# Kernel optimization log

Hardware: AMD Instinct MI355X
Metric: run time of the kernel (lower is better)

Reference implementation:

```python
import jax, jax.numpy as jnp
import numpy as np

B, T = 2048, 512
H1, H2, H3 = 100, 60, 30


def _glorot(key, shape, fan):
    bound = 1.0 / np.sqrt(fan)
    return jax.random.uniform(key, shape, jnp.float32, -bound, bound)


def setup_inputs() -> dict:
    key = jax.random.key(0)
    ks = jax.random.split(key, 17)
    inp = {"x": jax.random.normal(ks[0], (B, T, 2), jnp.float32)}
    # layer 1: input 2 -> hidden 100
    inp["W_ih1"] = _glorot(ks[1], (H1, 2), H1)
    inp["W_hh1"] = _glorot(ks[2], (H1, H1), H1)
    inp["b_ih1"] = _glorot(ks[3], (H1,), H1)
    inp["b_hh1"] = _glorot(ks[4], (H1,), H1)
    # layer 2: 100 -> 60
    inp["W_ih2"] = _glorot(ks[5], (H2, H1), H2)
    inp["W_hh2"] = _glorot(ks[6], (H2, H2), H2)
    inp["b_ih2"] = _glorot(ks[7], (H2,), H2)
    inp["b_hh2"] = _glorot(ks[8], (H2,), H2)
    # layer 3: 60 -> 30
    inp["W_ih3"] = _glorot(ks[9], (H3, H2), H3)
    inp["W_hh3"] = _glorot(ks[10], (H3, H3), H3)
    inp["b_ih3"] = _glorot(ks[11], (H3,), H3)
    inp["b_hh3"] = _glorot(ks[12], (H3,), H3)
    # heads
    inp["W_o1"] = _glorot(ks[13], (10, H3), 10)
    inp["b_o1"] = _glorot(ks[14], (10,), 10)
    inp["W_o2"] = _glorot(ks[15], (2, 10), 2)
    inp["b_o2"] = _glorot(ks[16], (2,), 2)
    return inp


def rnn_layer(x, W_ih, W_hh, b_ih, b_hh):
    # x: [B, T, in]; precompute the time-parallel input projection once
    xp = jnp.einsum("bti,hi->bth", x, W_ih) + (b_ih + b_hh)  # [B, T, H]
    h0 = jnp.zeros((x.shape[0], W_hh.shape[0]), x.dtype)

    def step(h, xt):  # xt: [B, H]
        h = jnp.tanh(xt + h @ W_hh.T)
        return h, h

    _, ys = jax.lax.scan(step, h0, jnp.swapaxes(xp, 0, 1))  # [T, B, H]
    return jnp.swapaxes(ys, 0, 1)  # [B, T, H]


def reference(x, W_ih1, W_hh1, b_ih1, b_hh1, W_ih2, W_hh2, b_ih2, b_hh2,
              W_ih3, W_hh3, b_ih3, b_hh3, W_o1, b_o1, W_o2, b_o2):
    h = rnn_layer(x, W_ih1, W_hh1, b_ih1, b_hh1)
    h = rnn_layer(h, W_ih2, W_hh2, b_ih2, b_hh2)
    h = rnn_layer(h, W_ih3, W_hh3, b_ih3, b_hh3)
    o = jnp.einsum("bth,oh->bto", h, W_o1) + b_o1
    return jnp.einsum("bto,po->btp", o, W_o2) + b_o2  # [B, T, 2]
```

## Files before the change

### kernel.cpp

```cpp
#include <hip/hip_runtime.h>

typedef _Float16 v8hf __attribute__((ext_vector_type(8)));
typedef float    v4f  __attribute__((ext_vector_type(4)));

#define MFMA16(a, b, c) __builtin_amdgcn_mfma_f32_16x16x32_f16((a), (b), (c), 0, 0, 0)

#define TT 512
#define BT 16
#define NTH 512

#define PBLK  8192u
#define H2OFF 4352u
#define H3OFF 6656u
#define XSTO  16384u
#define RINGO 49152u

__shared__ __align__(64) char SM[57344];

__device__ __forceinline__ v4f tanh4(v4f r) {
    const float KS = 2.8853900817779268f;
    const float CL = 13.8498724f;
    float z0 = __builtin_amdgcn_fmed3f(r[0] * KS, -CL, CL);
    float z1 = __builtin_amdgcn_fmed3f(r[1] * KS, -CL, CL);
    float z2 = __builtin_amdgcn_fmed3f(r[2] * KS, -CL, CL);
    float z3 = __builtin_amdgcn_fmed3f(r[3] * KS, -CL, CL);
    float a0 = __builtin_amdgcn_exp2f(z0) + 1.f;
    float a1 = __builtin_amdgcn_exp2f(z1) + 1.f;
    float a2 = __builtin_amdgcn_exp2f(z2) + 1.f;
    float a3 = __builtin_amdgcn_exp2f(z3) + 1.f;
    float P = a0 * a1, Q = a2 * a3;
    float R = __builtin_amdgcn_rcpf(P * Q);
    float iP = Q * R, iQ = P * R;
    v4f t;
    t[0] = 1.f - 2.f * (a1 * iP);
    t[1] = 1.f - 2.f * (a0 * iP);
    t[2] = 1.f - 2.f * (a3 * iQ);
    t[3] = 1.f - 2.f * (a2 * iQ);
    return t;
}

__global__ __launch_bounds__(NTH)
void rnn3_hl(const float* __restrict__ xg,
             const float* __restrict__ Wih1, const float* __restrict__ Whh1,
             const float* __restrict__ bih1, const float* __restrict__ bhh1,
             const float* __restrict__ Wih2, const float* __restrict__ Whh2,
             const float* __restrict__ bih2, const float* __restrict__ bhh2,
             const float* __restrict__ Wih3, const float* __restrict__ Whh3,
             const float* __restrict__ bih3, const float* __restrict__ bhh3,
             const float* __restrict__ Wo1,  const float* __restrict__ bo1,
             const float* __restrict__ Wo2,  const float* __restrict__ bo2,
             float* __restrict__ outg)
{
    const int tid   = threadIdx.x;
    const int lane  = tid & 63;
    const int wid   = tid >> 6;
    const int col   = lane & 15;
    const int g     = lane >> 4;
    const int bbase = blockIdx.x * BT;

    {
        float4 z = {0.f, 0.f, 0.f, 0.f};
        float4* p4 = (float4*)SM;
        for (int i = tid; i < 1024; i += NTH) p4[i] = z;
        for (int i = tid; i < BT * TT * 2; i += NTH) {
            float v = xg[(size_t)bbase * (TT * 2) + i];
            int b = i >> 10, r = i & 1023, t = r >> 1, c = r & 1;
            *(_Float16*)(SM + XSTO + (unsigned)t * 64u + (unsigned)b * 4u + (unsigned)c * 2u) = (_Float16)v;
        }
    }

    v8hf F[14];
    #pragma unroll
    for (int i = 0; i < 14; ++i) F[i] = (v8hf)(_Float16)0.f;
    float bb0 = 0.f, bb1 = 0.f, bb2 = 0.f;

    auto ldW = [&](const float* W, int rows, int cols, int j, int kt) -> v8hf {
        v8hf r;
        #pragma unroll
        for (int e = 0; e < 8; ++e) {
            const int k = kt * 32 + g * 8 + e;
            float v = (j < rows && k < cols) ? W[j * cols + k] : 0.f;
            r[e] = (_Float16)v;
        }
        return r;
    };
    auto ldW1 = [&](int j, int kt) -> v8hf {
        v8hf r;
        #pragma unroll
        for (int e = 0; e < 8; ++e) {
            const int k = kt * 32 + g * 8 + e;
            float v = 0.f;
            if (j < 100) {
                if (k < 100)       v = Whh1[j * 100 + k];
                else if (k == 112) v = Wih1[j * 2];
                else if (k == 113) v = Wih1[j * 2 + 1];
            }
            r[e] = (_Float16)v;
        }
        return r;
    };
    auto bL1 = [&](int j) -> float { return (j < 100) ? bih1[j] + bhh1[j] : 0.f; };
    auto bL2 = [&](int j) -> float { return (j < 60) ? bih2[j] + bhh2[j] : 0.f; };
    auto bL3 = [&](int j) -> float { return (j < 30) ? bih3[j] + bhh3[j] : 0.f; };

    unsigned oA = 0, oB = 0, oC = 0, oW1 = 0, oW2 = 0, oW3 = 0, oXw = 0, oRw = 0;

    if (wid < 4) {
        const int jA = 16 * wid + col;
        #pragma unroll
        for (int kt = 0; kt < 4; ++kt) {
            F[0 + kt] = ldW1(jA, kt);
            F[8 + kt] = ldW(Wih2, 60, 100, jA, kt);
        }
        F[12] = ldW(Whh2, 60, 60, jA, 0);
        F[13] = ldW(Whh2, 60, 60, jA, 1);
        bb0 = bL1(jA); bb2 = bL2(jA);
        if (wid < 3) {
            const int jB = jA + 64;
            #pragma unroll
            for (int kt = 0; kt < 4; ++kt) F[4 + kt] = ldW1(jB, kt);
            bb1 = bL1(jB);
        }
        oA  = (unsigned)col * 272u + (unsigned)g * 16u;
        oB  = PBLK + H2OFF + (unsigned)col * 144u + (unsigned)g * 16u;
        oW1 = PBLK + (unsigned)(4 * g) * 272u + (unsigned)jA * 2u;
        oW2 = H2OFF + (unsigned)(4 * g) * 144u + (unsigned)jA * 2u;
        oXw = PBLK + (unsigned)lane * 272u + 224u;
    } else if (wid < 6) {
        const int j3 = 16 * (wid - 4) + col;
        F[0] = ldW(Wih3, 30, 60, j3, 0);
        F[1] = ldW(Wih3, 30, 60, j3, 1);
        F[2] = ldW(Whh3, 30, 30, j3, 0);
        bb0 = bL3(j3);
        oB  = PBLK + H2OFF + (unsigned)col * 144u + (unsigned)g * 16u;
        oC  = H3OFF + (unsigned)col * 80u + (unsigned)g * 16u;
        oW3 = PBLK + H3OFF + (unsigned)(4 * g) * 80u + (unsigned)j3 * 2u;
    } else if (wid == 6) {
        #pragma unroll
        for (int e = 0; e < 8; ++e) {
            const int k = g * 8 + e;
            float v = 0.f;
            if (col < 2 && k < 30) {
                #pragma unroll
                for (int u = 0; u < 10; ++u) v += Wo2[col * 10 + u] * Wo1[u * 30 + k];
            }
            F[0][e] = (_Float16)v;
        }
        if (col < 2) {
            float bv = bo2[col];
            #pragma unroll
            for (int u = 0; u < 10; ++u) bv += Wo2[col * 10 + u] * bo1[u];
            bb0 = bv;
        }
        oC  = H3OFF + (unsigned)col * 80u + (unsigned)g * 16u;
        oRw = RINGO + (unsigned)(4 * g) * 512u + (unsigned)col * 4u;
    }

    __syncthreads();
    if (tid < BT)
        *(unsigned*)(SM + (unsigned)tid * 272u + 224u) =
            *(const unsigned*)(SM + XSTO + (unsigned)tid * 4u);
    __syncthreads();

#define ST_H1(r, EX) { \
    *(_Float16*)(SM + oW1 + (EX) + 0u)   = (_Float16)(r)[0]; \
    *(_Float16*)(SM + oW1 + (EX) + 272u) = (_Float16)(r)[1]; \
    *(_Float16*)(SM + oW1 + (EX) + 544u) = (_Float16)(r)[2]; \
    *(_Float16*)(SM + oW1 + (EX) + 816u) = (_Float16)(r)[3]; }
#define ST_H2(r) { \
    *(_Float16*)(SM + oW2 + 0u)   = (_Float16)(r)[0]; \
    *(_Float16*)(SM + oW2 + 144u) = (_Float16)(r)[1]; \
    *(_Float16*)(SM + oW2 + 288u) = (_Float16)(r)[2]; \
    *(_Float16*)(SM + oW2 + 432u) = (_Float16)(r)[3]; }
#define ST_H3(r) { \
    *(_Float16*)(SM + oW3 + 0u)   = (_Float16)(r)[0]; \
    *(_Float16*)(SM + oW3 + 80u)  = (_Float16)(r)[1]; \
    *(_Float16*)(SM + oW3 + 160u) = (_Float16)(r)[2]; \
    *(_Float16*)(SM + oW3 + 240u) = (_Float16)(r)[3]; }

    for (int s = 0; s < TT + 4; ++s) {
        if (wid < 4) {
            if (wid == 3 && lane < BT && s < TT - 1) {
                unsigned xv = *(const unsigned*)(SM + XSTO + (unsigned)(s + 1) * 64u + (unsigned)lane * 4u);
                *(unsigned*)(SM + oXw) = xv;
            }
            if (s <= TT) {
                v8hf A0 = *(const v8hf*)(SM + oA);
                v8hf A1 = *(const v8hf*)(SM + oA + 64u);
                v8hf A2 = *(const v8hf*)(SM + oA + 128u);
                v8hf A3 = *(const v8hf*)(SM + oA + 192u);
                v8hf B0 = *(const v8hf*)(SM + oB);
                v8hf B1 = *(const v8hf*)(SM + oB + 64u);
                if (s < TT) {
                    {
                        v4f p = {bb0, bb0, bb0, bb0}, q = {0.f, 0.f, 0.f, 0.f};
                        p = MFMA16(A0, F[0], p); q = MFMA16(A1, F[1], q);
                        p = MFMA16(A2, F[2], p); q = MFMA16(A3, F[3], q);
                        v4f r = tanh4(p + q); ST_H1(r, 0u);
                    }
                    if (wid < 3) {
                        v4f p = {bb1, bb1, bb1, bb1}, q = {0.f, 0.f, 0.f, 0.f};
                        p = MFMA16(A0, F[4], p); q = MFMA16(A1, F[5], q);
                        p = MFMA16(A2, F[6], p); q = MFMA16(A3, F[7], q);
                        v4f r = tanh4(p + q); ST_H1(r, 128u);
                    }
                }
                if (s >= 1) {
                    v4f p = {bb2, bb2, bb2, bb2}, q = {0.f, 0.f, 0.f, 0.f};
                    p = MFMA16(A0, F[8],  p); q = MFMA16(A1, F[9],  q);
                    p = MFMA16(A2, F[10], p); q = MFMA16(A3, F[11], q);
                    p = MFMA16(B0, F[12], p); q = MFMA16(B1, F[13], q);
                    v4f r = tanh4(p + q); ST_H2(r);
                }
            }
            oA ^= PBLK; oB ^= PBLK; oW1 ^= PBLK; oW2 ^= PBLK; oXw ^= PBLK;
        } else if (wid < 6) {
            if (s >= 2 && s <= TT + 1) {
                v8hf B0 = *(const v8hf*)(SM + oB);
                v8hf B1 = *(const v8hf*)(SM + oB + 64u);
                v8hf C0 = *(const v8hf*)(SM + oC);
                v4f p = {bb0, bb0, bb0, bb0}, q = {0.f, 0.f, 0.f, 0.f};
                p = MFMA16(B0, F[0], p); q = MFMA16(B1, F[1], q);
                p = MFMA16(C0, F[2], p);
                v4f r = tanh4(p + q); ST_H3(r);
            }
            oB ^= PBLK; oC ^= PBLK; oW3 ^= PBLK;
        } else if (wid == 6) {
            if (s >= 3 && s <= TT + 2) {
                v8hf C0 = *(const v8hf*)(SM + oC);
                v4f o = {bb0, bb0, bb0, bb0};
                o = MFMA16(C0, F[0], o);
                const unsigned so = ((unsigned)(s - 3) & 63u) * 8u;
                if (col < 2) {
                    *(float*)(SM + oRw + so + 0u)    = o[0];
                    *(float*)(SM + oRw + so + 512u)  = o[1];
                    *(float*)(SM + oRw + so + 1024u) = o[2];
                    *(float*)(SM + oRw + so + 1536u) = o[3];
                }
            }
            oC ^= PBLK;
        } else {
            if (s >= 35 && ((s - 4) & 31) == 31) {
                const int tbase = s - 35;
                const unsigned rb = RINGO + (((unsigned)tbase & 63u) >> 1) * 16u;
                #pragma unroll
                for (int jj = 0; jj < 4; ++jj) {
                    const int f = lane + 64 * jj;
                    const int b = f >> 4, k = f & 15;
                    float4 v = *(const float4*)(SM + rb + (unsigned)b * 512u + (unsigned)k * 16u);
                    *(float4*)(outg + ((size_t)(bbase + b) * TT + tbase) * 2 + 4 * k) = v;
                }
            }
        }
        __syncthreads();
    }
}

extern "C" void kernel_launch(void* const* d_in, const int* in_sizes, int n_in,
                              void* d_out, int out_size, void* d_ws, size_t ws_size,
                              hipStream_t stream) {
    (void)in_sizes; (void)n_in; (void)d_ws; (void)ws_size; (void)out_size;
    const float* x     = (const float*)d_in[0];
    const float* W_ih1 = (const float*)d_in[1];
    const float* W_hh1 = (const float*)d_in[2];
    const float* b_ih1 = (const float*)d_in[3];
    const float* b_hh1 = (const float*)d_in[4];
    const float* W_ih2 = (const float*)d_in[5];
    const float* W_hh2 = (const float*)d_in[6];
    const float* b_ih2 = (const float*)d_in[7];
    const float* b_hh2 = (const float*)d_in[8];
    const float* W_ih3 = (const float*)d_in[9];
    const float* W_hh3 = (const float*)d_in[10];
    const float* b_ih3 = (const float*)d_in[11];
    const float* b_hh3 = (const float*)d_in[12];
    const float* W_o1  = (const float*)d_in[13];
    const float* b_o1  = (const float*)d_in[14];
    const float* W_o2  = (const float*)d_in[15];
    const float* b_o2  = (const float*)d_in[16];
    float* out = (float*)d_out;

    rnn3_hl<<<2048 / BT, NTH, 0, stream>>>(
        x, W_ih1, W_hh1, b_ih1, b_hh1,
        W_ih2, W_hh2, b_ih2, b_hh2,
        W_ih3, W_hh3, b_ih3, b_hh3,
        W_o1, b_o1, W_o2, b_o2, out);
}
```

Before: 311.5 us.

## Specialise time loop into unrolled ping-pong phases and prioritise layer-1/2 waves

The 516-step time loop is unrolled by two with compile-time buffer parity, and prologue/epilogue steps are split out so per-step conditionals and pointer XORs disappear. The x-staging copy moves from wave 3 (on the critical layer-1 path) to the head wave 6. Waves running layers 1 and 2 get raised scheduling priority via s_setprio. This trades larger code size and more register pressure for less per-step scalar and branch overhead on the serial recurrence.

```diff
diff --git a/kernel.cpp b/kernel.cpp
--- a/kernel.cpp
+++ b/kernel.cpp
@@ -40,7 +40,7 @@
 }
 
 __global__ __launch_bounds__(NTH)
-void rnn3_hl(const float* __restrict__ xg,
+void rnn3_sp(const float* __restrict__ xg,
              const float* __restrict__ Wih1, const float* __restrict__ Whh1,
              const float* __restrict__ bih1, const float* __restrict__ bhh1,
              const float* __restrict__ Wih2, const float* __restrict__ Whh2,
@@ -103,7 +103,8 @@
     auto bL2 = [&](int j) -> float { return (j < 60) ? bih2[j] + bhh2[j] : 0.f; };
     auto bL3 = [&](int j) -> float { return (j < 30) ? bih3[j] + bhh3[j] : 0.f; };
 
-    unsigned oA = 0, oB = 0, oC = 0, oW1 = 0, oW2 = 0, oW3 = 0, oXw = 0, oRw = 0;
+    unsigned bRd = 0, bRd2 = 0, bRd3 = 0, bW1 = 0, bW2 = 0, bW3 = 0, bXw = 0, bRw = 0;
+    unsigned xr = 0;
 
     if (wid < 4) {
         const int jA = 16 * wid + col;
@@ -121,20 +122,19 @@
             for (int kt = 0; kt < 4; ++kt) F[4 + kt] = ldW1(jB, kt);
             bb1 = bL1(jB);
         }
-        oA  = (unsigned)col * 272u + (unsigned)g * 16u;
-        oB  = PBLK + H2OFF + (unsigned)col * 144u + (unsigned)g * 16u;
-        oW1 = PBLK + (unsigned)(4 * g) * 272u + (unsigned)jA * 2u;
-        oW2 = H2OFF + (unsigned)(4 * g) * 144u + (unsigned)jA * 2u;
-        oXw = PBLK + (unsigned)lane * 272u + 224u;
+        bRd  = (unsigned)col * 272u + (unsigned)g * 16u;
+        bRd2 = (unsigned)col * 144u + (unsigned)g * 16u;
+        bW1  = (unsigned)(4 * g) * 272u + (unsigned)jA * 2u;
+        bW2  = (unsigned)(4 * g) * 144u + (unsigned)jA * 2u;
     } else if (wid < 6) {
         const int j3 = 16 * (wid - 4) + col;
         F[0] = ldW(Wih3, 30, 60, j3, 0);
         F[1] = ldW(Wih3, 30, 60, j3, 1);
         F[2] = ldW(Whh3, 30, 30, j3, 0);
         bb0 = bL3(j3);
-        oB  = PBLK + H2OFF + (unsigned)col * 144u + (unsigned)g * 16u;
-        oC  = H3OFF + (unsigned)col * 80u + (unsigned)g * 16u;
-        oW3 = PBLK + H3OFF + (unsigned)(4 * g) * 80u + (unsigned)j3 * 2u;
+        bRd2 = (unsigned)col * 144u + (unsigned)g * 16u;
+        bRd3 = (unsigned)col * 80u + (unsigned)g * 16u;
+        bW3  = (unsigned)(4 * g) * 80u + (unsigned)j3 * 2u;
     } else if (wid == 6) {
         #pragma unroll
         for (int e = 0; e < 8; ++e) {
@@ -152,8 +152,10 @@
             for (int u = 0; u < 10; ++u) bv += Wo2[col * 10 + u] * bo1[u];
             bb0 = bv;
         }
-        oC  = H3OFF + (unsigned)col * 80u + (unsigned)g * 16u;
-        oRw = RINGO + (unsigned)(4 * g) * 512u + (unsigned)col * 4u;
+        bRd3 = (unsigned)col * 80u + (unsigned)g * 16u;
+        bXw  = (unsigned)lane * 272u + 224u;
+        xr   = XSTO + 64u + (unsigned)lane * 4u;
+        bRw  = RINGO + (unsigned)(4 * g) * 512u + (unsigned)col * 4u;
     }
 
     __syncthreads();
@@ -162,98 +164,116 @@
             *(const unsigned*)(SM + XSTO + (unsigned)tid * 4u);
     __syncthreads();
 
-#define ST_H1(r, EX) { \
-    *(_Float16*)(SM + oW1 + (EX) + 0u)   = (_Float16)(r)[0]; \
-    *(_Float16*)(SM + oW1 + (EX) + 272u) = (_Float16)(r)[1]; \
-    *(_Float16*)(SM + oW1 + (EX) + 544u) = (_Float16)(r)[2]; \
-    *(_Float16*)(SM + oW1 + (EX) + 816u) = (_Float16)(r)[3]; }
-#define ST_H2(r) { \
-    *(_Float16*)(SM + oW2 + 0u)   = (_Float16)(r)[0]; \
-    *(_Float16*)(SM + oW2 + 144u) = (_Float16)(r)[1]; \
-    *(_Float16*)(SM + oW2 + 288u) = (_Float16)(r)[2]; \
-    *(_Float16*)(SM + oW2 + 432u) = (_Float16)(r)[3]; }
-#define ST_H3(r) { \
-    *(_Float16*)(SM + oW3 + 0u)   = (_Float16)(r)[0]; \
-    *(_Float16*)(SM + oW3 + 80u)  = (_Float16)(r)[1]; \
-    *(_Float16*)(SM + oW3 + 160u) = (_Float16)(r)[2]; \
-    *(_Float16*)(SM + oW3 + 240u) = (_Float16)(r)[3]; }
-
-    for (int s = 0; s < TT + 4; ++s) {
-        if (wid < 4) {
-            if (wid == 3 && lane < BT && s < TT - 1) {
-                unsigned xv = *(const unsigned*)(SM + XSTO + (unsigned)(s + 1) * 64u + (unsigned)lane * 4u);
-                *(unsigned*)(SM + oXw) = xv;
-            }
-            if (s <= TT) {
-                v8hf A0 = *(const v8hf*)(SM + oA);
-                v8hf A1 = *(const v8hf*)(SM + oA + 64u);
-                v8hf A2 = *(const v8hf*)(SM + oA + 128u);
-                v8hf A3 = *(const v8hf*)(SM + oA + 192u);
-                v8hf B0 = *(const v8hf*)(SM + oB);
-                v8hf B1 = *(const v8hf*)(SM + oB + 64u);
-                if (s < TT) {
-                    {
-                        v4f p = {bb0, bb0, bb0, bb0}, q = {0.f, 0.f, 0.f, 0.f};
-                        p = MFMA16(A0, F[0], p); q = MFMA16(A1, F[1], q);
-                        p = MFMA16(A2, F[2], p); q = MFMA16(A3, F[3], q);
-                        v4f r = tanh4(p + q); ST_H1(r, 0u);
-                    }
-                    if (wid < 3) {
-                        v4f p = {bb1, bb1, bb1, bb1}, q = {0.f, 0.f, 0.f, 0.f};
-                        p = MFMA16(A0, F[4], p); q = MFMA16(A1, F[5], q);
-                        p = MFMA16(A2, F[6], p); q = MFMA16(A3, F[7], q);
-                        v4f r = tanh4(p + q); ST_H1(r, 128u);
-                    }
-                }
-                if (s >= 1) {
-                    v4f p = {bb2, bb2, bb2, bb2}, q = {0.f, 0.f, 0.f, 0.f};
-                    p = MFMA16(A0, F[8],  p); q = MFMA16(A1, F[9],  q);
-                    p = MFMA16(A2, F[10], p); q = MFMA16(A3, F[11], q);
-                    p = MFMA16(B0, F[12], p); q = MFMA16(B1, F[13], q);
-                    v4f r = tanh4(p + q); ST_H2(r);
-                }
-            }
-            oA ^= PBLK; oB ^= PBLK; oW1 ^= PBLK; oW2 ^= PBLK; oXw ^= PBLK;
-        } else if (wid < 6) {
-            if (s >= 2 && s <= TT + 1) {
-                v8hf B0 = *(const v8hf*)(SM + oB);
-                v8hf B1 = *(const v8hf*)(SM + oB + 64u);
-                v8hf C0 = *(const v8hf*)(SM + oC);
-                v4f p = {bb0, bb0, bb0, bb0}, q = {0.f, 0.f, 0.f, 0.f};
-                p = MFMA16(B0, F[0], p); q = MFMA16(B1, F[1], q);
-                p = MFMA16(C0, F[2], p);
-                v4f r = tanh4(p + q); ST_H3(r);
-            }
-            oB ^= PBLK; oC ^= PBLK; oW3 ^= PBLK;
-        } else if (wid == 6) {
-            if (s >= 3 && s <= TT + 2) {
-                v8hf C0 = *(const v8hf*)(SM + oC);
-                v4f o = {bb0, bb0, bb0, bb0};
-                o = MFMA16(C0, F[0], o);
-                const unsigned so = ((unsigned)(s - 3) & 63u) * 8u;
-                if (col < 2) {
-                    *(float*)(SM + oRw + so + 0u)    = o[0];
-                    *(float*)(SM + oRw + so + 512u)  = o[1];
-                    *(float*)(SM + oRw + so + 1024u) = o[2];
-                    *(float*)(SM + oRw + so + 1536u) = o[3];
-                }
-            }
-            oC ^= PBLK;
-        } else {
-            if (s >= 35 && ((s - 4) & 31) == 31) {
-                const int tbase = s - 35;
-                const unsigned rb = RINGO + (((unsigned)tbase & 63u) >> 1) * 16u;
-                #pragma unroll
-                for (int jj = 0; jj < 4; ++jj) {
-                    const int f = lane + 64 * jj;
-                    const int b = f >> 4, k = f & 15;
-                    float4 v = *(const float4*)(SM + rb + (unsigned)b * 512u + (unsigned)k * 16u);
-                    *(float4*)(outg + ((size_t)(bbase + b) * TT + tbase) * 2 + 4 * k) = v;
-                }
-            }
-        }
-        __syncthreads();
+    if (wid < 4) __builtin_amdgcn_s_setprio(1);
+
+    auto flushfn = [&](int s) {
+        const int tbase = s - 35;
+        const unsigned rb = RINGO + (((unsigned)tbase & 63u) >> 1) * 16u;
+        #pragma unroll
+        for (int jj = 0; jj < 4; ++jj) {
+            const int f = lane + 64 * jj;
+            const int b = f >> 4, k = f & 15;
+            float4 v = *(const float4*)(SM + rb + (unsigned)b * 512u + (unsigned)k * 16u);
+            *(float4*)(outg + ((size_t)(bbase + b) * TT + tbase) * 2 + 4 * k) = v;
+        }
+    };
+
+#define PHASE(RP, L1ON, L2ON, L3ON, HDON, XON, S) do {                                   \
+    const unsigned RB_ = (RP) ? PBLK : 0u;                                               \
+    const unsigned WB_ = (RP) ? 0u : PBLK;                                               \
+    if (wid < 4) {                                                                       \
+        if ((L1ON) || (L2ON)) {                                                          \
+            v8hf A0 = *(const v8hf*)(SM + bRd + RB_ + 0u);                               \
+            v8hf A1 = *(const v8hf*)(SM + bRd + RB_ + 64u);                              \
+            v8hf A2 = *(const v8hf*)(SM + bRd + RB_ + 128u);                             \
+            v8hf A3 = *(const v8hf*)(SM + bRd + RB_ + 192u);                             \
+            if (L1ON) {                                                                  \
+                { v4f p = {bb0, bb0, bb0, bb0}, q = {0.f, 0.f, 0.f, 0.f};                \
+                  p = MFMA16(A0, F[0], p); q = MFMA16(A1, F[1], q);                      \
+                  p = MFMA16(A2, F[2], p); q = MFMA16(A3, F[3], q);                      \
+                  v4f r = tanh4(p + q);                                                  \
+                  *(_Float16*)(SM + bW1 + WB_ + 0u)   = (_Float16)r[0];                  \
+                  *(_Float16*)(SM + bW1 + WB_ + 272u) = (_Float16)r[1];                  \
+                  *(_Float16*)(SM + bW1 + WB_ + 544u) = (_Float16)r[2];                  \
+                  *(_Float16*)(SM + bW1 + WB_ + 816u) = (_Float16)r[3]; }                \
+                if (wid < 3) {                                                           \
+                  v4f p = {bb1, bb1, bb1, bb1}, q = {0.f, 0.f, 0.f, 0.f};                \
+                  p = MFMA16(A0, F[4], p); q = MFMA16(A1, F[5], q);                      \
+                  p = MFMA16(A2, F[6], p); q = MFMA16(A3, F[7], q);                      \
+                  v4f r = tanh4(p + q);                                                  \
+                  *(_Float16*)(SM + bW1 + WB_ + 128u)  = (_Float16)r[0];                 \
+                  *(_Float16*)(SM + bW1 + WB_ + 400u)  = (_Float16)r[1];                 \
+                  *(_Float16*)(SM + bW1 + WB_ + 672u)  = (_Float16)r[2];                 \
+                  *(_Float16*)(SM + bW1 + WB_ + 944u)  = (_Float16)r[3]; }               \
+            }                                                                            \
+            if (L2ON) {                                                                  \
+                v8hf B0 = *(const v8hf*)(SM + bRd2 + WB_ + H2OFF + 0u);                  \
+                v8hf B1 = *(const v8hf*)(SM + bRd2 + WB_ + H2OFF + 64u);                 \
+                v4f p = {bb2, bb2, bb2, bb2}, q = {0.f, 0.f, 0.f, 0.f};                  \
+                p = MFMA16(A0, F[8],  p); q = MFMA16(A1, F[9],  q);                      \
+                p = MFMA16(A2, F[10], p); q = MFMA16(A3, F[11], q);                      \
+                p = MFMA16(B0, F[12], p); q = MFMA16(B1, F[13], q);                      \
+                v4f r = tanh4(p + q);                                                    \
+                *(_Float16*)(SM + bW2 + RB_ + H2OFF + 0u)   = (_Float16)r[0];            \
+                *(_Float16*)(SM + bW2 + RB_ + H2OFF + 144u) = (_Float16)r[1];            \
+                *(_Float16*)(SM + bW2 + RB_ + H2OFF + 288u) = (_Float16)r[2];            \
+                *(_Float16*)(SM + bW2 + RB_ + H2OFF + 432u) = (_Float16)r[3];            \
+            }                                                                            \
+        }                                                                                \
+    } else if (wid < 6) {                                                                \
+        if (L3ON) {                                                                      \
+            v8hf B0 = *(const v8hf*)(SM + bRd2 + WB_ + H2OFF + 0u);                      \
+            v8hf B1 = *(const v8hf*)(SM + bRd2 + WB_ + H2OFF + 64u);                     \
+            v8hf C0 = *(const v8hf*)(SM + bRd3 + RB_ + H3OFF);                           \
+            v4f p = {bb0, bb0, bb0, bb0}, q = {0.f, 0.f, 0.f, 0.f};                      \
+            p = MFMA16(B0, F[0], p); q = MFMA16(B1, F[1], q);                            \
+            p = MFMA16(C0, F[2], p);                                                     \
+            v4f r = tanh4(p + q);                                                        \
+            *(_Float16*)(SM + bW3 + WB_ + H3OFF + 0u)   = (_Float16)r[0];                \
+            *(_Float16*)(SM + bW3 + WB_ + H3OFF + 80u)  = (_Float16)r[1];                \
+            *(_Float16*)(SM + bW3 + WB_ + H3OFF + 160u) = (_Float16)r[2];                \
+            *(_Float16*)(SM + bW3 + WB_ + H3OFF + 240u) = (_Float16)r[3];                \
+        }                                                                                \
+    } else if (wid == 6) {                                                               \
+        if (XON) {                                                                       \
+            if (lane < 16) {                                                             \
+                unsigned xv = *(const unsigned*)(SM + xr);                               \
+                *(unsigned*)(SM + bXw + WB_) = xv;                                       \
+            }                                                                            \
+        }                                                                                \
+        xr += 64u;                                                                       \
+        if (HDON) {                                                                      \
+            v8hf C0 = *(const v8hf*)(SM + bRd3 + RB_ + H3OFF);                           \
+            v4f o = {bb0, bb0, bb0, bb0};                                                \
+            o = MFMA16(C0, F[0], o);                                                     \
+            const unsigned so = (((unsigned)(S) - 3u) & 63u) * 8u;                       \
+            if (col < 2) {                                                               \
+                *(float*)(SM + bRw + so + 0u)    = o[0];                                 \
+                *(float*)(SM + bRw + so + 512u)  = o[1];                                 \
+                *(float*)(SM + bRw + so + 1024u) = o[2];                                 \
+                *(float*)(SM + bRw + so + 1536u) = o[3];                                 \
+            }                                                                            \
+        }                                                                                \
+    } else {                                                                             \
+        if ((S) >= 35 && (((S) - 4) & 31) == 31) flushfn((S));                           \
+    }                                                                                    \
+    __syncthreads();                                                                     \
+} while (0)
+
+    PHASE(0, 1, 0, 0, 0, 1, 0);
+    PHASE(1, 1, 1, 0, 0, 1, 1);
+    PHASE(0, 1, 1, 1, 0, 1, 2);
+    PHASE(1, 1, 1, 1, 1, 1, 3);
+    for (int s = 4; s < 510; s += 2) {
+        PHASE(0, 1, 1, 1, 1, 1, s);
+        PHASE(1, 1, 1, 1, 1, 1, s + 1);
     }
+    PHASE(0, 1, 1, 1, 1, 1, 510);
+    PHASE(1, 1, 1, 1, 1, 0, 511);
+    PHASE(0, 0, 1, 1, 1, 0, 512);
+    PHASE(1, 0, 0, 1, 1, 0, 513);
+    PHASE(0, 0, 0, 0, 1, 0, 514);
+    PHASE(1, 0, 0, 0, 0, 0, 515);
 }
 
 extern "C" void kernel_launch(void* const* d_in, const int* in_sizes, int n_in,
@@ -279,7 +299,7 @@
     const float* b_o2  = (const float*)d_in[16];
     float* out = (float*)d_out;
 
-    rnn3_hl<<<2048 / BT, NTH, 0, stream>>>(
+    rnn3_sp<<<2048 / BT, NTH, 0, stream>>>(
         x, W_ih1, W_hh1, b_ih1, b_hh1,
         W_ih2, W_hh2, b_ih2, b_hh2,
         W_ih3, W_hh3, b_ih3, b_hh3,
```

Result: no change. 307.5 us (-1.3%).

## Assign one wavefront per RNN layer with register-resident state and two-step barriers

Applied to the files above, without the earlier changes.

Restructures the kernel so each of four wavefronts owns one role: layer 1, layer 2, layer 3 plus the fused output head, and the output writer. Hidden state now stays in registers as MFMA B-operands, with the transposed MFMA operand order letting outputs pack straight into the next step's input. Each barrier covers two timesteps, using 4-deep shared rings between layers. The tanh scale factor is folded into the weights and biases. This cuts the block-wide barriers and shared-memory round trips on the recurrent path, but one wavefront now serially carries all 28 layer-1 MFMAs per step, which lengthens the critical path.

```diff
diff --git a/kernel.cpp b/kernel.cpp
--- a/kernel.cpp
+++ b/kernel.cpp
@@ -7,23 +7,23 @@
 
 #define TT 512
 #define BT 16
-#define NTH 512
-
-#define PBLK  8192u
-#define H2OFF 4352u
-#define H3OFF 6656u
-#define XSTO  16384u
-#define RINGO 49152u
-
-__shared__ __align__(64) char SM[57344];
-
-__device__ __forceinline__ v4f tanh4(v4f r) {
-    const float KS = 2.8853900817779268f;
-    const float CL = 13.8498724f;
-    float z0 = __builtin_amdgcn_fmed3f(r[0] * KS, -CL, CL);
-    float z1 = __builtin_amdgcn_fmed3f(r[1] * KS, -CL, CL);
-    float z2 = __builtin_amdgcn_fmed3f(r[2] * KS, -CL, CL);
-    float z3 = __builtin_amdgcn_fmed3f(r[3] * KS, -CL, CL);
+#define NTH 256
+#define KS 2.8853900817779268f
+#define CL 13.8498724f
+
+#define H1R 0u
+#define H2R 16384u
+#define XST 24576u
+#define ORG 57408u
+#define SMEMB 65600
+
+extern __shared__ __align__(16) char SM[];
+
+__device__ __forceinline__ v4f tanh4s(v4f z) {
+    float z0 = __builtin_amdgcn_fmed3f(z[0], -CL, CL);
+    float z1 = __builtin_amdgcn_fmed3f(z[1], -CL, CL);
+    float z2 = __builtin_amdgcn_fmed3f(z[2], -CL, CL);
+    float z3 = __builtin_amdgcn_fmed3f(z[3], -CL, CL);
     float a0 = __builtin_amdgcn_exp2f(z0) + 1.f;
     float a1 = __builtin_amdgcn_exp2f(z1) + 1.f;
     float a2 = __builtin_amdgcn_exp2f(z2) + 1.f;
@@ -39,8 +39,19 @@
     return t;
 }
 
-__global__ __launch_bounds__(NTH)
-void rnn3_hl(const float* __restrict__ xg,
+__device__ __forceinline__ unsigned pk2h(float a, float b) {
+    union { _Float16 h[2]; unsigned u; } x;
+    x.h[0] = (_Float16)a; x.h[1] = (_Float16)b;
+    return x.u;
+}
+__device__ __forceinline__ v8hf mk8(unsigned a, unsigned b, unsigned c, unsigned d) {
+    union { unsigned u[4]; v8hf h; } x;
+    x.u[0] = a; x.u[1] = b; x.u[2] = c; x.u[3] = d;
+    return x.h;
+}
+
+__global__ __launch_bounds__(NTH, 1)
+void rnn3_ws(const float* __restrict__ xg,
              const float* __restrict__ Wih1, const float* __restrict__ Whh1,
              const float* __restrict__ bih1, const float* __restrict__ bhh1,
              const float* __restrict__ Wih2, const float* __restrict__ Whh2,
@@ -58,191 +69,202 @@
     const int g     = lane >> 4;
     const int bbase = blockIdx.x * BT;
 
-    {
-        float4 z = {0.f, 0.f, 0.f, 0.f};
-        float4* p4 = (float4*)SM;
-        for (int i = tid; i < 1024; i += NTH) p4[i] = z;
-        for (int i = tid; i < BT * TT * 2; i += NTH) {
-            float v = xg[(size_t)bbase * (TT * 2) + i];
-            int b = i >> 10, r = i & 1023, t = r >> 1, c = r & 1;
-            *(_Float16*)(SM + XSTO + (unsigned)t * 64u + (unsigned)b * 4u + (unsigned)c * 2u) = (_Float16)v;
-        }
+    for (int i = tid; i < BT * TT; i += NTH) {
+        const int b = i >> 9, t = i & 511;
+        float2 xv = *(const float2*)(xg + (size_t)(bbase + b) * (TT * 2) + 2 * t);
+        *(unsigned*)(SM + XST + (unsigned)t * 64u + (unsigned)b * 4u) = pk2h(xv.x, xv.y);
     }
-
-    v8hf F[14];
-    #pragma unroll
-    for (int i = 0; i < 14; ++i) F[i] = (v8hf)(_Float16)0.f;
-    float bb0 = 0.f, bb1 = 0.f, bb2 = 0.f;
-
-    auto ldW = [&](const float* W, int rows, int cols, int j, int kt) -> v8hf {
+    if (tid < 16) *(unsigned*)(SM + XST + 512u * 64u + (unsigned)tid * 4u) = 0u;
+    __syncthreads();
+
+    auto ldA = [&](const float* W, int rows, int cols, int jg, int kt) -> v8hf {
         v8hf r;
         #pragma unroll
         for (int e = 0; e < 8; ++e) {
-            const int k = kt * 32 + g * 8 + e;
-            float v = (j < rows && k < cols) ? W[j * cols + k] : 0.f;
+            const int kl = 32 * kt + 16 * (e >> 2) + 4 * g + (e & 3);
+            float v = (jg < rows && kl < cols) ? W[jg * cols + kl] * KS : 0.f;
             r[e] = (_Float16)v;
         }
         return r;
     };
-    auto ldW1 = [&](int j, int kt) -> v8hf {
+    auto ldA1 = [&](int jg, int kt) -> v8hf {
         v8hf r;
         #pragma unroll
         for (int e = 0; e < 8; ++e) {
-            const int k = kt * 32 + g * 8 + e;
+            const int kl = 32 * kt + 16 * (e >> 2) + 4 * g + (e & 3);
             float v = 0.f;
-            if (j < 100) {
-                if (k < 100)       v = Whh1[j * 100 + k];
-                else if (k == 112) v = Wih1[j * 2];
-                else if (k == 113) v = Wih1[j * 2 + 1];
-            }
-            r[e] = (_Float16)v;
+            if (jg < 100) {
+                if (kl < 100)       v = Whh1[jg * 100 + kl];
+                else if (kl == 112) v = Wih1[jg * 2];
+                else if (kl == 113) v = Wih1[jg * 2 + 1];
+            }
+            r[e] = (_Float16)(v * KS);
         }
         return r;
     };
-    auto bL1 = [&](int j) -> float { return (j < 100) ? bih1[j] + bhh1[j] : 0.f; };
-    auto bL2 = [&](int j) -> float { return (j < 60) ? bih2[j] + bhh2[j] : 0.f; };
-    auto bL3 = [&](int j) -> float { return (j < 30) ? bih3[j] + bhh3[j] : 0.f; };
-
-    unsigned oA = 0, oB = 0, oC = 0, oW1 = 0, oW2 = 0, oW3 = 0, oXw = 0, oRw = 0;
-
-    if (wid < 4) {
-        const int jA = 16 * wid + col;
-        #pragma unroll
-        for (int kt = 0; kt < 4; ++kt) {
-            F[0 + kt] = ldW1(jA, kt);
-            F[8 + kt] = ldW(Wih2, 60, 100, jA, kt);
-        }
-        F[12] = ldW(Whh2, 60, 60, jA, 0);
-        F[13] = ldW(Whh2, 60, 60, jA, 1);
-        bb0 = bL1(jA); bb2 = bL2(jA);
-        if (wid < 3) {
-            const int jB = jA + 64;
-            #pragma unroll
-            for (int kt = 0; kt < 4; ++kt) F[4 + kt] = ldW1(jB, kt);
-            bb1 = bL1(jB);
-        }
-        oA  = (unsigned)col * 272u + (unsigned)g * 16u;
-        oB  = PBLK + H2OFF + (unsigned)col * 144u + (unsigned)g * 16u;
-        oW1 = PBLK + (unsigned)(4 * g) * 272u + (unsigned)jA * 2u;
-        oW2 = H2OFF + (unsigned)(4 * g) * 144u + (unsigned)jA * 2u;
-        oXw = PBLK + (unsigned)lane * 272u + 224u;
-    } else if (wid < 6) {
-        const int j3 = 16 * (wid - 4) + col;
-        F[0] = ldW(Wih3, 30, 60, j3, 0);
-        F[1] = ldW(Wih3, 30, 60, j3, 1);
-        F[2] = ldW(Whh3, 30, 30, j3, 0);
-        bb0 = bL3(j3);
-        oB  = PBLK + H2OFF + (unsigned)col * 144u + (unsigned)g * 16u;
-        oC  = H3OFF + (unsigned)col * 80u + (unsigned)g * 16u;
-        oW3 = PBLK + H3OFF + (unsigned)(4 * g) * 80u + (unsigned)j3 * 2u;
-    } else if (wid == 6) {
+    auto mkbias = [&](const float* bi, const float* bh, int n, int t) -> v4f {
+        v4f b;
+        #pragma unroll
+        for (int i = 0; i < 4; ++i) {
+            const int j = 16 * t + 4 * g + i;
+            b[i] = (j < n) ? KS * (bi[j] + bh[j]) : 0.f;
+        }
+        return b;
+    };
+
+    const v8hf z8 = (v8hf)(_Float16)0.f;
+
+    if (wid == 0) {
+        v8hf W1f[7][4]; v4f B1[7];
+        #pragma unroll
+        for (int t = 0; t < 7; ++t) {
+            #pragma unroll
+            for (int kt = 0; kt < 4; ++kt) W1f[t][kt] = ldA1(16 * t + col, kt);
+            B1[t] = mkbias(bih1, bhh1, 100, t);
+        }
+        v8hf H0 = z8, H1 = z8, H2 = z8, H3;
+        {
+            unsigned x0 = *(const unsigned*)(SM + XST + (unsigned)col * 4u);
+            H3 = mk8(0u, 0u, (g == 0) ? x0 : 0u, 0u);
+        }
+        for (int u = 0; u <= 258; ++u) {
+            #pragma unroll
+            for (int sub = 0; sub < 2; ++sub) {
+                const int s = 2 * u + sub;
+                if (s < TT) {
+                    unsigned xn = 0u;
+                    if (s < TT - 1)
+                        xn = *(const unsigned*)(SM + XST + (unsigned)(s + 1) * 64u + (unsigned)col * 4u);
+                    unsigned lo[7], hi[7];
+                    #pragma unroll
+                    for (int t = 0; t < 7; ++t) {
+                        v4f p = B1[t];
+                        p = MFMA16(W1f[t][0], H0, p);
+                        p = MFMA16(W1f[t][1], H1, p);
+                        p = MFMA16(W1f[t][2], H2, p);
+                        p = MFMA16(W1f[t][3], H3, p);
+                        v4f r = tanh4s(p);
+                        lo[t] = pk2h(r[0], r[1]); hi[t] = pk2h(r[2], r[3]);
+                    }
+                    H0 = mk8(lo[0], hi[0], lo[1], hi[1]);
+                    H1 = mk8(lo[2], hi[2], lo[3], hi[3]);
+                    H2 = mk8(lo[4], hi[4], lo[5], hi[5]);
+                    H3 = mk8(lo[6], hi[6], (g == 0) ? xn : 0u, 0u);
+                    char* wb = SM + H1R + (unsigned)(s & 3) * 4096u + (unsigned)lane * 16u;
+                    *(v8hf*)(wb)        = H0;
+                    *(v8hf*)(wb + 1024) = H1;
+                    *(v8hf*)(wb + 2048) = H2;
+                    *(v8hf*)(wb + 3072) = H3;
+                }
+            }
+            __syncthreads();
+        }
+    } else if (wid == 1) {
+        v8hf Wi2[4][4], Wh2[4][2]; v4f B2[4];
+        #pragma unroll
+        for (int t = 0; t < 4; ++t) {
+            #pragma unroll
+            for (int kt = 0; kt < 4; ++kt) Wi2[t][kt] = ldA(Wih2, 60, 100, 16 * t + col, kt);
+            Wh2[t][0] = ldA(Whh2, 60, 60, 16 * t + col, 0);
+            Wh2[t][1] = ldA(Whh2, 60, 60, 16 * t + col, 1);
+            B2[t] = mkbias(bih2, bhh2, 60, t);
+        }
+        v8hf Sa = z8, Sb = z8;
+        for (int u = 0; u <= 258; ++u) {
+            #pragma unroll
+            for (int sub = 0; sub < 2; ++sub) {
+                const int s1 = 2 * u + sub - 2;
+                if (s1 >= 0 && s1 < TT) {
+                    const char* rb = SM + H1R + (unsigned)(s1 & 3) * 4096u + (unsigned)lane * 16u;
+                    v8hf G0 = *(const v8hf*)(rb);
+                    v8hf G1 = *(const v8hf*)(rb + 1024);
+                    v8hf G2 = *(const v8hf*)(rb + 2048);
+                    v8hf G3 = *(const v8hf*)(rb + 3072);
+                    unsigned lo[4], hi[4];
+                    #pragma unroll
+                    for (int t = 0; t < 4; ++t) {
+                        v4f p = B2[t];
+                        p = MFMA16(Wi2[t][0], G0, p);
+                        p = MFMA16(Wi2[t][1], G1, p);
+                        p = MFMA16(Wi2[t][2], G2, p);
+                        p = MFMA16(Wi2[t][3], G3, p);
+                        p = MFMA16(Wh2[t][0], Sa, p);
+                        p = MFMA16(Wh2[t][1], Sb, p);
+                        v4f r = tanh4s(p);
+                        lo[t] = pk2h(r[0], r[1]); hi[t] = pk2h(r[2], r[3]);
+                    }
+                    Sa = mk8(lo[0], hi[0], lo[1], hi[1]);
+                    Sb = mk8(lo[2], hi[2], lo[3], hi[3]);
+                    char* wb = SM + H2R + (unsigned)(s1 & 3) * 2048u + (unsigned)lane * 16u;
+                    *(v8hf*)(wb)        = Sa;
+                    *(v8hf*)(wb + 1024) = Sb;
+                }
+            }
+            __syncthreads();
+        }
+    } else if (wid == 2) {
+        v8hf Wi3[2][2], Wh3[2], We; v4f B3[2], Bh;
+        #pragma unroll
+        for (int t = 0; t < 2; ++t) {
+            Wi3[t][0] = ldA(Wih3, 30, 60, 16 * t + col, 0);
+            Wi3[t][1] = ldA(Wih3, 30, 60, 16 * t + col, 1);
+            Wh3[t]    = ldA(Whh3, 30, 30, 16 * t + col, 0);
+            B3[t] = mkbias(bih3, bhh3, 30, t);
+        }
         #pragma unroll
         for (int e = 0; e < 8; ++e) {
-            const int k = g * 8 + e;
+            const int kl = 16 * (e >> 2) + 4 * g + (e & 3);
             float v = 0.f;
-            if (col < 2 && k < 30) {
+            if (col < 2 && kl < 30) {
                 #pragma unroll
-                for (int u = 0; u < 10; ++u) v += Wo2[col * 10 + u] * Wo1[u * 30 + k];
-            }
-            F[0][e] = (_Float16)v;
-        }
-        if (col < 2) {
-            float bv = bo2[col];
-            #pragma unroll
-            for (int u = 0; u < 10; ++u) bv += Wo2[col * 10 + u] * bo1[u];
-            bb0 = bv;
-        }
-        oC  = H3OFF + (unsigned)col * 80u + (unsigned)g * 16u;
-        oRw = RINGO + (unsigned)(4 * g) * 512u + (unsigned)col * 4u;
-    }
-
-    __syncthreads();
-    if (tid < BT)
-        *(unsigned*)(SM + (unsigned)tid * 272u + 224u) =
-            *(const unsigned*)(SM + XSTO + (unsigned)tid * 4u);
-    __syncthreads();
-
-#define ST_H1(r, EX) { \
-    *(_Float16*)(SM + oW1 + (EX) + 0u)   = (_Float16)(r)[0]; \
-    *(_Float16*)(SM + oW1 + (EX) + 272u) = (_Float16)(r)[1]; \
-    *(_Float16*)(SM + oW1 + (EX) + 544u) = (_Float16)(r)[2]; \
-    *(_Float16*)(SM + oW1 + (EX) + 816u) = (_Float16)(r)[3]; }
-#define ST_H2(r) { \
-    *(_Float16*)(SM + oW2 + 0u)   = (_Float16)(r)[0]; \
-    *(_Float16*)(SM + oW2 + 144u) = (_Float16)(r)[1]; \
-    *(_Float16*)(SM + oW2 + 288u) = (_Float16)(r)[2]; \
-    *(_Float16*)(SM + oW2 + 432u) = (_Float16)(r)[3]; }
-#define ST_H3(r) { \
-    *(_Float16*)(SM + oW3 + 0u)   = (_Float16)(r)[0]; \
-    *(_Float16*)(SM + oW3 + 80u)  = (_Float16)(r)[1]; \
-    *(_Float16*)(SM + oW3 + 160u) = (_Float16)(r)[2]; \
-    *(_Float16*)(SM + oW3 + 240u) = (_Float16)(r)[3]; }
-
-    for (int s = 0; s < TT + 4; ++s) {
-        if (wid < 4) {
-            if (wid == 3 && lane < BT && s < TT - 1) {
-                unsigned xv = *(const unsigned*)(SM + XSTO + (unsigned)(s + 1) * 64u + (unsigned)lane * 4u);
-                *(unsigned*)(SM + oXw) = xv;
-            }
-            if (s <= TT) {
-                v8hf A0 = *(const v8hf*)(SM + oA);
-                v8hf A1 = *(const v8hf*)(SM + oA + 64u);
-                v8hf A2 = *(const v8hf*)(SM + oA + 128u);
-                v8hf A3 = *(const v8hf*)(SM + oA + 192u);
-                v8hf B0 = *(const v8hf*)(SM + oB);
-                v8hf B1 = *(const v8hf*)(SM + oB + 64u);
-                if (s < TT) {
-                    {
-                        v4f p = {bb0, bb0, bb0, bb0}, q = {0.f, 0.f, 0.f, 0.f};
-                        p = MFMA16(A0, F[0], p); q = MFMA16(A1, F[1], q);
-                        p = MFMA16(A2, F[2], p); q = MFMA16(A3, F[3], q);
-                        v4f r = tanh4(p + q); ST_H1(r, 0u);
+                for (int uu = 0; uu < 10; ++uu) v += Wo2[col * 10 + uu] * Wo1[uu * 30 + kl];
+            }
+            We[e] = (_Float16)v;
+        }
+        #pragma unroll
+        for (int i = 0; i < 4; ++i) {
+            float bv = 0.f;
+            if (g == 0 && i < 2) {
+                bv = bo2[i];
+                #pragma unroll
+                for (int uu = 0; uu < 10; ++uu) bv += Wo2[i * 10 + uu] * bo1[uu];
+            }
+            Bh[i] = bv;
+        }
+        v8hf S3 = z8;
+        for (int u = 0; u <= 258; ++u) {
+            #pragma unroll
+            for (int sub = 0; sub < 2; ++sub) {
+                const int s2 = 2 * u + sub - 4;
+                if (s2 >= 0 && s2 < TT) {
+                    const char* rb = SM + H2R + (unsigned)(s2 & 3) * 2048u + (unsigned)lane * 16u;
+                    v8hf G0 = *(const v8hf*)(rb);
+                    v8hf G1 = *(const v8hf*)(rb + 1024);
+                    unsigned lo[2], hi[2];
+                    #pragma unroll
+                    for (int t = 0; t < 2; ++t) {
+                        v4f p = B3[t];
+                        p = MFMA16(Wi3[t][0], G0, p);
+                        p = MFMA16(Wi3[t][1], G1, p);
+                        p = MFMA16(Wh3[t], S3, p);
+                        v4f r = tanh4s(p);
+                        lo[t] = pk2h(r[0], r[1]); hi[t] = pk2h(r[2], r[3]);
                     }
-                    if (wid < 3) {
-                        v4f p = {bb1, bb1, bb1, bb1}, q = {0.f, 0.f, 0.f, 0.f};
-                        p = MFMA16(A0, F[4], p); q = MFMA16(A1, F[5], q);
-                        p = MFMA16(A2, F[6], p); q = MFMA16(A3, F[7], q);
-                        v4f r = tanh4(p + q); ST_H1(r, 128u);
-                    }
+                    S3 = mk8(lo[0], hi[0], lo[1], hi[1]);
+                    v4f o = Bh;
+                    o = MFMA16(We, S3, o);
+                    if (g == 0)
+                        *(float2*)(SM + ORG + (unsigned)col * 512u + (unsigned)(s2 & 63) * 8u) =
+                            make_float2(o[0], o[1]);
                 }
-                if (s >= 1) {
-                    v4f p = {bb2, bb2, bb2, bb2}, q = {0.f, 0.f, 0.f, 0.f};
-                    p = MFMA16(A0, F[8],  p); q = MFMA16(A1, F[9],  q);
-                    p = MFMA16(A2, F[10], p); q = MFMA16(A3, F[11], q);
-                    p = MFMA16(B0, F[12], p); q = MFMA16(B1, F[13], q);
-                    v4f r = tanh4(p + q); ST_H2(r);
-                }
-            }
-            oA ^= PBLK; oB ^= PBLK; oW1 ^= PBLK; oW2 ^= PBLK; oXw ^= PBLK;
-        } else if (wid < 6) {
-            if (s >= 2 && s <= TT + 1) {
-                v8hf B0 = *(const v8hf*)(SM + oB);
-                v8hf B1 = *(const v8hf*)(SM + oB + 64u);
-                v8hf C0 = *(const v8hf*)(SM + oC);
-                v4f p = {bb0, bb0, bb0, bb0}, q = {0.f, 0.f, 0.f, 0.f};
-                p = MFMA16(B0, F[0], p); q = MFMA16(B1, F[1], q);
-                p = MFMA16(C0, F[2], p);
-                v4f r = tanh4(p + q); ST_H3(r);
-            }
-            oB ^= PBLK; oC ^= PBLK; oW3 ^= PBLK;
-        } else if (wid == 6) {
-            if (s >= 3 && s <= TT + 2) {
-                v8hf C0 = *(const v8hf*)(SM + oC);
-                v4f o = {bb0, bb0, bb0, bb0};
-                o = MFMA16(C0, F[0], o);
-                const unsigned so = ((unsigned)(s - 3) & 63u) * 8u;
-                if (col < 2) {
-                    *(float*)(SM + oRw + so + 0u)    = o[0];
-                    *(float*)(SM + oRw + so + 512u)  = o[1];
-                    *(float*)(SM + oRw + so + 1024u) = o[2];
-                    *(float*)(SM + oRw + so + 1536u) = o[3];
-                }
-            }
-            oC ^= PBLK;
-        } else {
-            if (s >= 35 && ((s - 4) & 31) == 31) {
-                const int tbase = s - 35;
-                const unsigned rb = RINGO + (((unsigned)tbase & 63u) >> 1) * 16u;
+            }
+            __syncthreads();
+        }
+    } else {
+        for (int u = 0; u <= 258; ++u) {
+            if (u >= 18 && ((u - 18) & 15) == 0) {
+                const int tbase = 2 * u - 36;
+                const unsigned rb = ORG + (((unsigned)tbase & 63u) >> 1) * 16u;
                 #pragma unroll
                 for (int jj = 0; jj < 4; ++jj) {
                     const int f = lane + 64 * jj;
@@ -251,8 +273,8 @@
                     *(float4*)(outg + ((size_t)(bbase + b) * TT + tbase) * 2 + 4 * k) = v;
                 }
             }
-        }
-        __syncthreads();
+            __syncthreads();
+        }
     }
 }
 
@@ -279,7 +301,9 @@
     const float* b_o2  = (const float*)d_in[16];
     float* out = (float*)d_out;
 
-    rnn3_hl<<<2048 / BT, NTH, 0, stream>>>(
+    hipFuncSetAttribute((const void*)rnn3_ws,
+                        hipFuncAttributeMaxDynamicSharedMemorySize, SMEMB);
+    rnn3_ws<<<2048 / BT, NTH, SMEMB, stream>>>(
         x, W_ih1, W_hh1, b_ih1, b_hh1,
         W_ih2, W_hh2, b_ih2, b_hh2,
         W_ih3, W_hh3, b_ih3, b_hh3,
```

Result: slower. 406.3 us (+30.4%).
